# Kernel optimization log

Measured on AMD Instinct MI355X. Metric: run time of the kernel, lower is better.

## Reference

```python
import jax, jax.numpy as jnp
import numpy as np
from jax import lax

DIM = 180
NUM_HEADS = 6
WS = 16                     # window_size
OWS = 24                    # overlap_win_size = int(16 * 1.5)
PAD = (OWS - WS) // 2       # 4
EPS = 1e-5


def setup_inputs() -> dict:
    key = jax.random.key(0)
    ks = jax.random.split(key, 4)
    B, H, W, C = 1, 256, 256, DIM
    x = jax.random.normal(ks[0], (B, H * W, C), dtype=jnp.float32)
    s = 0.05  # keep logits in a sane range
    return {
        "x": x,
        "norm_w": jnp.ones((C,), jnp.float32),
        "norm_b": jnp.zeros((C,), jnp.float32),
        "q_w": jax.random.normal(ks[1], (C, C), jnp.float32) * s,
        "q_b": jnp.zeros((C,), jnp.float32),
        "kv_w": jax.random.normal(ks[2], (C, 2 * C), jnp.float32) * s,
        "kv_b": jnp.zeros((2 * C,), jnp.float32),
        "proj_w": jax.random.normal(ks[3], (C, C), jnp.float32) * s,
        "proj_b": jnp.zeros((C,), jnp.float32),
        "H": H,
        "W": W,
    }


def _ocab(x, norm_w, norm_b, q_w, q_b, kv_w, kv_b, proj_w, proj_b, H, W):
    B, N, C = x.shape
    nh, hd = NUM_HEADS, C // NUM_HEADS
    scale = hd ** (-0.5)
    nHw, nWw = H // WS, W // WS
    nW = nHw * nWw

    shortcut = x
    # LayerNorm
    mu = jnp.mean(x, axis=-1, keepdims=True)
    var = jnp.var(x, axis=-1, keepdims=True)
    xn = (x - mu) * lax.rsqrt(var + EPS) * norm_w + norm_b

    feat = xn.reshape(B, H, W, C)

    # --- query: non-overlapping window partition -> [B*nW, WS*WS, C]
    qw = feat.reshape(B, nHw, WS, nWw, WS, C).transpose(0, 1, 3, 2, 4, 5)
    qw = qw.reshape(B * nW, WS * WS, C)
    q = qw @ q_w + q_b

    # --- key/value: overlapping windows via unfold (kernel=OWS, stride=WS, pad=PAD)
    feat_chw = feat.transpose(0, 3, 1, 2)  # [B, C, H, W]
    patches = lax.conv_general_dilated_patches(
        feat_chw, filter_shape=(OWS, OWS), window_strides=(WS, WS),
        padding=((PAD, PAD), (PAD, PAD)))  # [B, C*OWS*OWS, nHw, nWw], channel-major
    kv_feat = patches.reshape(B, C, OWS * OWS, nW).transpose(0, 3, 2, 1)
    kv_feat = kv_feat.reshape(B * nW, OWS * OWS, C)
    kv = kv_feat @ kv_w + kv_b
    k, v = jnp.split(kv, 2, axis=-1)

    # --- multi-head attention: 256 queries vs 576 keys per window
    q = q.reshape(B * nW, WS * WS, nh, hd).transpose(0, 2, 1, 3)
    k = k.reshape(B * nW, OWS * OWS, nh, hd).transpose(0, 2, 1, 3)
    v = v.reshape(B * nW, OWS * OWS, nh, hd).transpose(0, 2, 1, 3)

    attn = jnp.einsum('whqd,whkd->whqk', q, k) * scale
    attn = jax.nn.softmax(attn, axis=-1)
    out = jnp.einsum('whqk,whkd->whqd', attn, v)
    out = out.transpose(0, 2, 1, 3).reshape(B * nW, WS * WS, C)
    out = out @ proj_w + proj_b

    # --- window reverse + residual
    out = out.reshape(B, nHw, nWw, WS, WS, C).transpose(0, 1, 3, 2, 4, 5)
    out = out.reshape(B, N, C)
    return shortcut + out


def reference(x, norm_w, norm_b, q_w, q_b, kv_w, kv_b, proj_w, proj_b, H, W):
    return _ocab(x, norm_w, norm_b, q_w, q_b, kv_w, kv_b, proj_w, proj_b, H, W)
```

## Files before the change

### kernel.cpp

```cpp
#include <hip/hip_runtime.h>
#include <math.h>

typedef __bf16 bf16x8 __attribute__((ext_vector_type(8)));
typedef float f32x4 __attribute__((ext_vector_type(4)));
typedef unsigned short ushort_t;

static __device__ __forceinline__ unsigned short f2bf(float f) {
  union { float f; unsigned int u; } c; c.f = f;
  unsigned int u = c.u;
  unsigned int r = u + 0x7FFFu + ((u >> 16) & 1u);
  return (unsigned short)(r >> 16);
}

#define CDIM 180
#define CPAD 192
#define NTOK 65536

#define SCL2E 0.26339361f

static __device__ __forceinline__ unsigned pk_bf(float a, float b) {
  union { float f; unsigned u; } ca, cb; ca.f = a; cb.f = b;
  return __builtin_amdgcn_perm(cb.u, ca.u, 0x07060302u);
}

__global__ __launch_bounds__(256) void prep_k(
    const float* __restrict__ q_w, const float* __restrict__ q_b,
    const float* __restrict__ kv_w, const float* __restrict__ kv_b,
    const float* __restrict__ p_w, const float* __restrict__ p_b,
    ushort_t* __restrict__ wqkvt, ushort_t* __restrict__ pwt,
    float* __restrict__ qkvb, float* __restrict__ pbp,
    ushort_t* __restrict__ k_bias_row, ushort_t* __restrict__ vt4_bias_grp)
{
  int i = blockIdx.x * 256 + threadIdx.x;
  if (i < 110592) {
    int n = i / 192, k = i % 192;
    float v = 0.f;
    if (k < CDIM) {
      if (n < 192) { int h = n >> 5, d = n & 31; if (d < 30) v = q_w[k * CDIM + h * 30 + d] * SCL2E; }
      else { int cn = n - 192; int part = cn >= 192; int c2 = cn - part * 192;
             int h = c2 >> 5, d = c2 & 31;
             if (d < 30) v = kv_w[k * 360 + part * 180 + h * 30 + d]; }
    }
    wqkvt[i] = f2bf(v);
    return;
  }
  i -= 110592;
  if (i < 36864) {
    int n = i / 192, r = i % 192, h = r >> 5, d = r & 31;
    float v = (d < 30 && n < CDIM) ? p_w[(h * 30 + d) * CDIM + n] : 0.f;
    pwt[i] = f2bf(v);
    return;
  }
  i -= 36864;
  if (i < 576) {
    float v = 0.f;
    if (i < 192) { int h = i >> 5, d = i & 31; if (d < 30) v = q_b[h * 30 + d] * SCL2E; }
    else { int cn = i - 192; int part = cn >= 192; int c2 = cn - part * 192;
           int h = c2 >> 5, d = c2 & 31;
           if (d < 30) v = kv_b[part * 180 + h * 30 + d];
           else if (part == 1 && d == 30) v = 1.0f; }
    qkvb[i] = v;
    return;
  }
  i -= 576;
  if (i < 192) { pbp[i] = (i < CDIM) ? p_b[i] : 0.f; return; }
  i -= 192;
  if (i < 192) {
    int h = i >> 5, d = i & 31;
    k_bias_row[i] = (d < 30) ? f2bf(kv_b[h * 30 + d]) : (ushort_t)0;
    return;
  }
  i -= 192;
  if (i < 768) {
    int d = i >> 2, h = d >> 5, dd = d & 31;
    float v = 0.f;
    if (dd < 30) v = kv_b[180 + h * 30 + dd];
    else if (dd == 30) v = 1.0f;
    vt4_bias_grp[i] = f2bf(v);
    return;
  }
}

__global__ __launch_bounds__(256) void ln_k(const float* __restrict__ x,
    const float* __restrict__ nw, const float* __restrict__ nb,
    ushort_t* __restrict__ xn)
{
  const int lane = threadIdx.x & 63, wave = threadIdx.x >> 6;
  const int row = blockIdx.x * 4 + wave;
  const float* xr = x + (size_t)row * CDIM;
  float f0 = xr[lane];
  float f1 = xr[lane + 64];
  float f2 = (lane < 52) ? xr[lane + 128] : 0.f;
  float sum = f0 + f1 + f2;
  float sq = f0 * f0 + f1 * f1 + f2 * f2;
  #pragma unroll
  for (int off = 1; off < 64; off <<= 1) {
    sum += __shfl_xor(sum, off, 64);
    sq  += __shfl_xor(sq, off, 64);
  }
  const float inv_n = 1.0f / 180.0f;
  float mean = sum * inv_n;
  float var = sq * inv_n - mean * mean;
  float rs = rsqrtf(var + 1e-5f);
  ushort_t* xo = xn + (size_t)row * CPAD;
  #pragma unroll
  for (int e = 0; e < 3; ++e) {
    int col = lane + e * 64;
    float v = 0.f;
    if (col < CDIM) v = (( (e==0)?f0 : (e==1)?f1 : f2 ) - mean) * rs * nw[col] + nb[col];
    xo[col] = f2bf(v);
  }
}

template<int MODE>
__global__ __launch_bounds__(256) void gemm_k(const ushort_t* __restrict__ A,
    const ushort_t* __restrict__ Wt, const float* __restrict__ bias,
    ushort_t* __restrict__ q_out, ushort_t* __restrict__ k_out,
    ushort_t* __restrict__ vt_out,
    float* __restrict__ outf, const float* __restrict__ resid)
{
  constexpr int NT = (MODE == 0) ? 9 : 3;
  __shared__ __align__(16) ushort_t aS[128 * 200];
  const int tid = threadIdx.x;
  const int lane = tid & 63, wave = tid >> 6;
  const int quad = lane >> 4, l16 = lane & 15;
  const int wm = wave & 1, wn = wave >> 1;
  const int bm = blockIdx.x;

  {
    const ushort_t* Ab = A + (size_t)bm * 128 * 192;
    #pragma unroll
    for (int it = 0; it < 12; ++it) {
      int f = it * 256 + tid;
      int row = f / 24, kq = f % 24;
      uint4 v = *reinterpret_cast<const uint4*>(Ab + row * 192 + kq * 8);
      *reinterpret_cast<uint4*>(&aS[row * 200 + kq * 8]) = v;
    }
  }
  __syncthreads();

  for (int nt0 = 0; nt0 < NT; ++nt0) {
    f32x4 acc[4][2] = {};
    #pragma unroll
    for (int ks = 0; ks < 6; ++ks) {
      bf16x8 af[4], bfr[2];
      #pragma unroll
      for (int nt = 0; nt < 2; ++nt) {
        int n = nt0 * 64 + wn * 32 + nt * 16 + l16;
        bfr[nt] = *reinterpret_cast<const bf16x8*>(Wt + (size_t)n * 192 + ks * 32 + quad * 8);
      }
      #pragma unroll
      for (int mt = 0; mt < 4; ++mt)
        af[mt] = *reinterpret_cast<const bf16x8*>(&aS[(wm * 64 + mt * 16 + l16) * 200 + ks * 32 + quad * 8]);
      #pragma unroll
      for (int mt = 0; mt < 4; ++mt)
        #pragma unroll
        for (int nt = 0; nt < 2; ++nt)
          acc[mt][nt] = __builtin_amdgcn_mfma_f32_16x16x32_bf16(af[mt], bfr[nt], acc[mt][nt], 0, 0, 0);
    }
    #pragma unroll
    for (int mt = 0; mt < 4; ++mt) {
      int row = bm * 128 + wm * 64 + mt * 16 + quad * 4;
      #pragma unroll
      for (int nt = 0; nt < 2; ++nt) {
        int ncol = nt0 * 64 + wn * 32 + nt * 16 + l16;
        float bv = bias[ncol];
        if (MODE == 0 && nt0 >= 6) {
          int d = ncol - 384;
          unsigned p0 = pk_bf(acc[mt][nt][0] + bv, acc[mt][nt][1] + bv);
          unsigned p1 = pk_bf(acc[mt][nt][2] + bv, acc[mt][nt][3] + bv);
          uint2 val; val.x = p0; val.y = p1;
          *reinterpret_cast<uint2*>(vt_out + (size_t)row * 192 + d * 4) = val;
        } else {
          #pragma unroll
          for (int r = 0; r < 4; ++r) {
            int rr = row + r;
            float v = acc[mt][nt][r] + bv;
            if (MODE == 0) {
              if (ncol < 192) q_out[(size_t)rr * CPAD + ncol] = f2bf(v);
              else k_out[(size_t)rr * CPAD + (ncol - 192)] = f2bf(v);
            } else {
              if (ncol < CDIM) outf[(size_t)rr * CDIM + ncol] = v + resid[(size_t)rr * CDIM + ncol];
            }
          }
        }
      }
    }
  }
}

__global__ __launch_bounds__(256, 4) void attn_k(const ushort_t* __restrict__ q_tok,
    const ushort_t* __restrict__ k_tok, const ushort_t* __restrict__ vt4,
    ushort_t* __restrict__ ao)
{
  const int w = blockIdx.x, h = blockIdx.y;
  const int tid = threadIdx.x;
  const int lane = tid & 63, wave = tid >> 6;
  const int quad = lane >> 4, l16 = lane & 15;
  const int wy = w >> 4, wx = w & 15;
  const int tok0 = wy * 16 * 256 + wx * 16;
  const int hc = h * 32;
  const int ybase = wy * 16 - 4, xbase = wx * 16 - 4;

  bf16x8 qf[4];
  #pragma unroll
  for (int qt = 0; qt < 4; ++qt) {
    int qi = wave * 64 + qt * 16 + l16;
    int token = tok0 + (qi >> 4) * 256 + (qi & 15);
    qf[qt] = *reinterpret_cast<const bf16x8*>(q_tok + (size_t)token * CPAD + hc + quad * 8);
  }

  const int key0 = ((l16 >> 2) << 3) + (l16 & 3);

  f32x4 o[4][2] = {};
  f32x4 zero = {0.f, 0.f, 0.f, 0.f};

  auto compute = [&](const bf16x8* kf, const uint2* va, const uint2* vb) {
    bf16x8 vf0, vf1;
    {
      union { unsigned u[4]; bf16x8 v; } a_;
      a_.u[0] = va[0].x; a_.u[1] = va[0].y; a_.u[2] = va[1].x; a_.u[3] = va[1].y;
      vf0 = a_.v;
      a_.u[0] = vb[0].x; a_.u[1] = vb[0].y; a_.u[2] = vb[1].x; a_.u[3] = vb[1].y;
      vf1 = a_.v;
    }
    __builtin_amdgcn_s_setprio(1);
    #pragma unroll
    for (int qt = 0; qt < 4; ++qt) {
      f32x4 s0 = __builtin_amdgcn_mfma_f32_16x16x32_bf16(kf[0], qf[qt], zero, 0, 0, 0);
      f32x4 s1 = __builtin_amdgcn_mfma_f32_16x16x32_bf16(kf[1], qf[qt], zero, 0, 0, 0);
      union { unsigned u[4]; bf16x8 v; } pk;
      pk.u[0] = pk_bf(__builtin_amdgcn_exp2f(s0[0]), __builtin_amdgcn_exp2f(s0[1]));
      pk.u[1] = pk_bf(__builtin_amdgcn_exp2f(s0[2]), __builtin_amdgcn_exp2f(s0[3]));
      pk.u[2] = pk_bf(__builtin_amdgcn_exp2f(s1[0]), __builtin_amdgcn_exp2f(s1[1]));
      pk.u[3] = pk_bf(__builtin_amdgcn_exp2f(s1[2]), __builtin_amdgcn_exp2f(s1[3]));
      o[qt][0] = __builtin_amdgcn_mfma_f32_16x16x32_bf16(pk.v, vf0, o[qt][0], 0, 0, 0);
      o[qt][1] = __builtin_amdgcn_mfma_f32_16x16x32_bf16(pk.v, vf1, o[qt][1], 0, 0, 0);
    }
    __builtin_amdgcn_s_setprio(0);
  };

  const bool interior = ((unsigned)(wy - 1) < 14u) && ((unsigned)(wx - 1) < 14u);

  if (interior) {
    unsigned koff[3][2], voff[3][2];
    #pragma unroll
    for (int cm = 0; cm < 3; ++cm) {
      #pragma unroll
      for (int j = 0; j < 2; ++j) {
        int pk = 32 * cm + key0 + 4 * j;
        int py = pk / 24, px = pk - py * 24;
        koff[cm][j] = (unsigned)((((ybase + py) * 256 + xbase + px) * 384) + (hc + quad * 8) * 2);
        int pv = 32 * cm + quad * 8 + 4 * j;
        int pyv = pv / 24, pxv = pv - pyv * 24;
        voff[cm][j] = (unsigned)((((ybase + pyv) * 256 + xbase + pxv) * 384) + (hc + l16) * 8);
      }
    }
    const char* kp = (const char*)k_tok;
    const char* vp = (const char*)vt4;
    auto lK = [&](int c, bf16x8* kf) {
      const int cm = c % 3; const unsigned cb = (unsigned)(c / 3) * 393216u;
      #pragma unroll
      for (int kt = 0; kt < 2; ++kt)
        kf[kt] = *reinterpret_cast<const bf16x8*>(kp + (size_t)(koff[cm][kt] + cb));
    };
    auto lV = [&](int c, uint2* va, uint2* vb) {
      const int cm = c % 3; const unsigned cb = (unsigned)(c / 3) * 393216u;
      #pragma unroll
      for (int h2 = 0; h2 < 2; ++h2) {
        const char* g = vp + (size_t)(voff[cm][h2] + cb);
        va[h2] = *reinterpret_cast<const uint2*>(g);
        vb[h2] = *reinterpret_cast<const uint2*>(g + 128);
      }
    };
    bf16x8 kbuf[3][2]; uint2 vabuf[3][2], vbbuf[3][2];
    lK(0, kbuf[0]); lV(0, vabuf[0], vbbuf[0]);
    lK(1, kbuf[1]); lV(1, vabuf[1], vbbuf[1]);
    #pragma unroll
    for (int c = 0; c < 18; ++c) {
      const int cur = c % 3, nxt = (c + 2) % 3;
      if (c < 16) { lK(c + 2, kbuf[nxt]); lV(c + 2, vabuf[nxt], vbbuf[nxt]); }
      compute(kbuf[cur], vabuf[cur], vbbuf[cur]);
    }
  } else {
    int kpy[3][2], ktx[3][2]; bool kxin[3][2];
    int vpy[3][2], vtx[3][2]; bool vxin[3][2];
    #pragma unroll
    for (int cm = 0; cm < 3; ++cm) {
      #pragma unroll
      for (int j = 0; j < 2; ++j) {
        int pk = 32 * cm + key0 + 4 * j;
        int py = pk / 24, px = pk - py * 24;
        kpy[cm][j] = py; ktx[cm][j] = xbase + px;
        kxin[cm][j] = (unsigned)(xbase + px) < 256u;
        int pv = 32 * cm + quad * 8 + 4 * j;
        int pyv = pv / 24, pxv = pv - pyv * 24;
        vpy[cm][j] = pyv; vtx[cm][j] = xbase + pxv;
        vxin[cm][j] = (unsigned)(xbase + pxv) < 256u;
      }
    }
    const int dOff0 = (hc + l16) * 4, dOff1 = (hc + 16 + l16) * 4;
    auto loadK = [&](int c, bf16x8* kf) {
      const int cm = c % 3, c3 = c / 3;
      const int yrow = ybase + 4 * c3;
      #pragma unroll
      for (int kt = 0; kt < 2; ++kt) {
        int y = yrow + kpy[cm][kt];
        bool inb = kxin[cm][kt] && ((unsigned)y < 256u);
        int t = inb ? (y * 256 + ktx[cm][kt]) : NTOK;
        kf[kt] = *reinterpret_cast<const bf16x8*>(k_tok + (size_t)t * CPAD + hc + quad * 8);
      }
    };
    auto loadV = [&](int c, uint2* va, uint2* vb) {
      const int cm = c % 3, c3 = c / 3;
      const int yrow = ybase + 4 * c3;
      #pragma unroll
      for (int h2 = 0; h2 < 2; ++h2) {
        int y = yrow + vpy[cm][h2];
        bool inb = vxin[cm][h2] && ((unsigned)y < 256u);
        int t = inb ? (y * 256 + vtx[cm][h2]) : NTOK;
        const ushort_t* gp = vt4 + (size_t)t * 192;
        va[h2] = *reinterpret_cast<const uint2*>(gp + dOff0);
        vb[h2] = *reinterpret_cast<const uint2*>(gp + dOff1);
      }
    };
    bf16x8 kbuf[2][2]; uint2 vabuf[2][2], vbbuf[2][2];
    loadK(0, kbuf[0]); loadV(0, vabuf[0], vbbuf[0]);
    #pragma unroll
    for (int c = 0; c < 18; ++c) {
      const int cur = c & 1, nxt = cur ^ 1;
      if (c < 17) { loadK(c + 1, kbuf[nxt]); loadV(c + 1, vabuf[nxt], vbbuf[nxt]); }
      compute(kbuf[cur], vabuf[cur], vbbuf[cur]);
    }
  }

  #pragma unroll
  for (int qt = 0; qt < 4; ++qt) {
    #pragma unroll
    for (int r = 0; r < 4; ++r) {
      float l = __shfl(o[qt][1][r], (lane & 48) + 14, 64);
      float inv = 1.0f / l;
      int qi = wave * 64 + qt * 16 + quad * 4 + r;
      int token = tok0 + (qi >> 4) * 256 + (qi & 15);
      ao[(size_t)token * CPAD + hc + l16]      = f2bf(o[qt][0][r] * inv);
      ao[(size_t)token * CPAD + hc + 16 + l16] = f2bf(o[qt][1][r] * inv);
    }
  }
}

extern "C" void kernel_launch(void* const* d_in, const int* in_sizes, int n_in,
                              void* d_out, int out_size, void* d_ws, size_t ws_size,
                              hipStream_t stream) {
  const float* x      = (const float*)d_in[0];
  const float* norm_w = (const float*)d_in[1];
  const float* norm_b = (const float*)d_in[2];
  const float* q_w    = (const float*)d_in[3];
  const float* q_b    = (const float*)d_in[4];
  const float* kv_w   = (const float*)d_in[5];
  const float* kv_b   = (const float*)d_in[6];
  const float* p_w    = (const float*)d_in[7];
  const float* p_b    = (const float*)d_in[8];

  char* base = (char*)d_ws;
  size_t off = 0;
  auto alloc = [&](size_t bytes) { char* p = base + off; off = (off + bytes + 255) & ~(size_t)255; return p; };
  ushort_t* xn_p  = (ushort_t*)alloc((size_t)NTOK * CPAD * 2);
  ushort_t* q_tok = (ushort_t*)alloc((size_t)NTOK * CPAD * 2);
  ushort_t* k_tok = (ushort_t*)alloc((size_t)(NTOK + 1) * CPAD * 2);
  ushort_t* vt4   = (ushort_t*)alloc((size_t)(NTOK + 4) * 192 * 2);
  ushort_t* wqkvt = (ushort_t*)alloc(576 * 192 * 2);
  ushort_t* pwt   = (ushort_t*)alloc(192 * 192 * 2);
  float* qkvb = (float*)alloc(576 * 4);
  float* pbp  = (float*)alloc(192 * 4);
  ushort_t* ao = xn_p;

  prep_k<<<583, 256, 0, stream>>>(q_w, q_b, kv_w, kv_b, p_w, p_b,
                                  wqkvt, pwt, qkvb, pbp,
                                  k_tok + (size_t)NTOK * CPAD,
                                  vt4 + (size_t)NTOK * 192);
  ln_k<<<NTOK / 4, 256, 0, stream>>>(x, norm_w, norm_b, xn_p);
  gemm_k<0><<<NTOK / 128, 256, 0, stream>>>(xn_p, wqkvt, qkvb, q_tok, k_tok, vt4, nullptr, nullptr);
  attn_k<<<dim3(256, 6), 256, 0, stream>>>(q_tok, k_tok, vt4, ao);
  gemm_k<1><<<NTOK / 128, 256, 0, stream>>>(ao, pwt, pbp, nullptr, nullptr, nullptr, (float*)d_out, x);
}
```

Baseline: 235.1 us.

## Fuse LayerNorm into the QKV GEMM prologue and drop the separate LN kernel

The standalone LayerNorm kernel is removed. The QKV GEMM (MODE 0) now reads the fp32 input rows directly, computes mean and variance with 16-lane shuffle reductions, applies the affine transform, and writes bf16 values straight into its shared-memory A tile, zero-filling the pad columns. This drops one kernel launch and the write and re-read of the padded bf16 normalized tensor in global memory. In exchange, each GEMM block does more serial prologue work before its MFMA loop, which may lengthen that phase.

```diff
diff --git a/kernel.cpp b/kernel.cpp
--- a/kernel.cpp
+++ b/kernel.cpp
@@ -81,39 +81,9 @@
   }
 }
 
-__global__ __launch_bounds__(256) void ln_k(const float* __restrict__ x,
-    const float* __restrict__ nw, const float* __restrict__ nb,
-    ushort_t* __restrict__ xn)
-{
-  const int lane = threadIdx.x & 63, wave = threadIdx.x >> 6;
-  const int row = blockIdx.x * 4 + wave;
-  const float* xr = x + (size_t)row * CDIM;
-  float f0 = xr[lane];
-  float f1 = xr[lane + 64];
-  float f2 = (lane < 52) ? xr[lane + 128] : 0.f;
-  float sum = f0 + f1 + f2;
-  float sq = f0 * f0 + f1 * f1 + f2 * f2;
-  #pragma unroll
-  for (int off = 1; off < 64; off <<= 1) {
-    sum += __shfl_xor(sum, off, 64);
-    sq  += __shfl_xor(sq, off, 64);
-  }
-  const float inv_n = 1.0f / 180.0f;
-  float mean = sum * inv_n;
-  float var = sq * inv_n - mean * mean;
-  float rs = rsqrtf(var + 1e-5f);
-  ushort_t* xo = xn + (size_t)row * CPAD;
-  #pragma unroll
-  for (int e = 0; e < 3; ++e) {
-    int col = lane + e * 64;
-    float v = 0.f;
-    if (col < CDIM) v = (( (e==0)?f0 : (e==1)?f1 : f2 ) - mean) * rs * nw[col] + nb[col];
-    xo[col] = f2bf(v);
-  }
-}
-
 template<int MODE>
 __global__ __launch_bounds__(256) void gemm_k(const ushort_t* __restrict__ A,
+    const float* __restrict__ x, const float* __restrict__ nw, const float* __restrict__ nb,
     const ushort_t* __restrict__ Wt, const float* __restrict__ bias,
     ushort_t* __restrict__ q_out, ushort_t* __restrict__ k_out,
     ushort_t* __restrict__ vt_out,
@@ -127,7 +97,65 @@
   const int wm = wave & 1, wn = wave >> 1;
   const int bm = blockIdx.x;
 
-  {
+  if constexpr (MODE == 0) {
+    const float* xb = x + (size_t)bm * 128 * CDIM;
+    const int grp = tid >> 4, gl = tid & 15;
+    float wv[12], bvv[12];
+    if (gl < 15) {
+      #pragma unroll
+      for (int e = 0; e < 3; ++e) {
+        float4 w4 = *reinterpret_cast<const float4*>(nw + gl * 12 + e * 4);
+        float4 b4 = *reinterpret_cast<const float4*>(nb + gl * 12 + e * 4);
+        wv[e*4+0] = w4.x; wv[e*4+1] = w4.y; wv[e*4+2] = w4.z; wv[e*4+3] = w4.w;
+        bvv[e*4+0] = b4.x; bvv[e*4+1] = b4.y; bvv[e*4+2] = b4.z; bvv[e*4+3] = b4.w;
+      }
+    } else {
+      #pragma unroll
+      for (int k = 0; k < 12; ++k) { wv[k] = 0.f; bvv[k] = 0.f; }
+    }
+    #pragma unroll 2
+    for (int i = 0; i < 8; ++i) {
+      const int row = i * 16 + grp;
+      const float* xr = xb + (size_t)row * CDIM;
+      float v[12];
+      float sum = 0.f, sq = 0.f;
+      if (gl < 15) {
+        #pragma unroll
+        for (int e = 0; e < 3; ++e) {
+          float4 x4 = *reinterpret_cast<const float4*>(xr + gl * 12 + e * 4);
+          v[e*4+0] = x4.x; v[e*4+1] = x4.y; v[e*4+2] = x4.z; v[e*4+3] = x4.w;
+        }
+        #pragma unroll
+        for (int k = 0; k < 12; ++k) { sum += v[k]; sq += v[k] * v[k]; }
+      } else {
+        #pragma unroll
+        for (int k = 0; k < 12; ++k) v[k] = 0.f;
+      }
+      #pragma unroll
+      for (int off = 1; off < 16; off <<= 1) {
+        sum += __shfl_xor(sum, off, 64);
+        sq  += __shfl_xor(sq, off, 64);
+      }
+      const float inv_n = 1.0f / 180.0f;
+      float mean = sum * inv_n;
+      float var = sq * inv_n - mean * mean;
+      float rs = rsqrtf(var + 1e-5f);
+      unsigned u[6];
+      #pragma unroll
+      for (int p = 0; p < 6; ++p) {
+        float a = (v[2*p]   - mean) * rs * wv[2*p]   + bvv[2*p];
+        float b = (v[2*p+1] - mean) * rs * wv[2*p+1] + bvv[2*p+1];
+        u[p] = (unsigned)f2bf(a) | ((unsigned)f2bf(b) << 16);
+      }
+      ushort_t* dst = &aS[row * 200 + gl * 12];
+      uint2 w01; w01.x = u[0]; w01.y = u[1];
+      uint2 w23; w23.x = u[2]; w23.y = u[3];
+      uint2 w45; w45.x = u[4]; w45.y = u[5];
+      *reinterpret_cast<uint2*>(dst)     = w01;
+      *reinterpret_cast<uint2*>(dst + 4) = w23;
+      *reinterpret_cast<uint2*>(dst + 8) = w45;
+    }
+  } else {
     const ushort_t* Ab = A + (size_t)bm * 128 * 192;
     #pragma unroll
     for (int it = 0; it < 12; ++it) {
@@ -364,7 +392,7 @@
   char* base = (char*)d_ws;
   size_t off = 0;
   auto alloc = [&](size_t bytes) { char* p = base + off; off = (off + bytes + 255) & ~(size_t)255; return p; };
-  ushort_t* xn_p  = (ushort_t*)alloc((size_t)NTOK * CPAD * 2);
+  ushort_t* ao    = (ushort_t*)alloc((size_t)NTOK * CPAD * 2);
   ushort_t* q_tok = (ushort_t*)alloc((size_t)NTOK * CPAD * 2);
   ushort_t* k_tok = (ushort_t*)alloc((size_t)(NTOK + 1) * CPAD * 2);
   ushort_t* vt4   = (ushort_t*)alloc((size_t)(NTOK + 4) * 192 * 2);
@@ -372,14 +400,14 @@
   ushort_t* pwt   = (ushort_t*)alloc(192 * 192 * 2);
   float* qkvb = (float*)alloc(576 * 4);
   float* pbp  = (float*)alloc(192 * 4);
-  ushort_t* ao = xn_p;
 
   prep_k<<<583, 256, 0, stream>>>(q_w, q_b, kv_w, kv_b, p_w, p_b,
                                   wqkvt, pwt, qkvb, pbp,
                                   k_tok + (size_t)NTOK * CPAD,
                                   vt4 + (size_t)NTOK * 192);
-  ln_k<<<NTOK / 4, 256, 0, stream>>>(x, norm_w, norm_b, xn_p);
-  gemm_k<0><<<NTOK / 128, 256, 0, stream>>>(xn_p, wqkvt, qkvb, q_tok, k_tok, vt4, nullptr, nullptr);
+  gemm_k<0><<<NTOK / 128, 256, 0, stream>>>(nullptr, x, norm_w, norm_b,
+                                            wqkvt, qkvb, q_tok, k_tok, vt4, nullptr, nullptr);
   attn_k<<<dim3(256, 6), 256, 0, stream>>>(q_tok, k_tok, vt4, ao);
-  gemm_k<1><<<NTOK / 128, 256, 0, stream>>>(ao, pwt, pbp, nullptr, nullptr, nullptr, (float*)d_out, x);
-}
+  gemm_k<1><<<NTOK / 128, 256, 0, stream>>>(ao, nullptr, nullptr, nullptr,
+                                            pwt, pbp, nullptr, nullptr, nullptr, (float*)d_out, x);
+}
```

Result: faster. 224.4 us (-4.6%).
